# Kernel optimization log

Hardware: AMD Instinct MI355X
Metric: run time of the kernel (lower is better)

Reference implementation:

```python
import jax, jax.numpy as jnp
import numpy as np

HIDDEN = 1024
HEADS = 16
HEAD_DIM = HIDDEN // HEADS  # 64
MLP_HIDDEN = int(HIDDEN * 4.0)  # 4096
B, L = 2, 2048
EPS_LN = 1e-6
EPS_RMS = 1e-6


def setup_inputs() -> dict:
    key = jax.random.key(0)
    ks = jax.random.split(key, 12)
    s = 0.02
    return {
        "x": jax.random.normal(ks[0], (B, L, HIDDEN), jnp.float32),
        "vec": jax.random.normal(ks[1], (B, HIDDEN), jnp.float32),
        "pe": jax.random.normal(ks[2], (1, 1, L, HEAD_DIM // 2, 2, 2), jnp.float32),
        "w_mod": jax.random.normal(ks[3], (HIDDEN, 3 * HIDDEN), jnp.float32) * s,
        "b_mod": jnp.zeros((3 * HIDDEN,), jnp.float32),
        "w1": jax.random.normal(ks[4], (HIDDEN, 3 * HIDDEN + MLP_HIDDEN), jnp.float32) * s,
        "b1": jnp.zeros((3 * HIDDEN + MLP_HIDDEN,), jnp.float32),
        "w_mlp": jax.random.normal(ks[5], (MLP_HIDDEN, HIDDEN), jnp.float32) * s,
        "b_mlp": jnp.zeros((HIDDEN,), jnp.float32),
        "w2": jax.random.normal(ks[6], (2 * HIDDEN, HIDDEN), jnp.float32) * s,
        "b2": jnp.zeros((HIDDEN,), jnp.float32),
        "q_scale": jnp.ones((HEAD_DIM,), jnp.float32),
        "k_scale": jnp.ones((HEAD_DIM,), jnp.float32),
    }


def _layernorm(x, eps=EPS_LN):
    m = jnp.mean(x, axis=-1, keepdims=True)
    v = jnp.mean(jnp.square(x - m), axis=-1, keepdims=True)
    return (x - m) * jax.lax.rsqrt(v + eps)


def _rmsnorm(x, scale, eps=EPS_RMS):
    rrms = jax.lax.rsqrt(jnp.mean(jnp.square(x), axis=-1, keepdims=True) + eps)
    return x * rrms * scale


def _apply_rope(t, pe):
    # t: [B,H,L,D]; pe: [1,1,L,D//2,2,2]
    t_ = t.reshape(*t.shape[:-1], -1, 1, 2)  # [B,H,L,D//2,1,2]
    out = pe[..., 0] * t_[..., 0] + pe[..., 1] * t_[..., 1]  # [B,H,L,D//2,2]
    return out.reshape(t.shape)


def reference(x, vec, pe, w_mod, b_mod, w1, b1, w_mlp, b_mlp, w2, b2, q_scale, k_scale):
    # adaLN modulation: silu(vec) -> Dense(3*dim) -> shift, scale, gate
    mod = (jax.nn.silu(vec) @ w_mod + b_mod)[:, None, :]  # [B,1,3H]
    shift, scale, gate = jnp.split(mod, 3, axis=-1)
    x_mod = (1.0 + scale) * _layernorm(x) + shift
    # fused QKV + MLP projection
    h = x_mod @ w1 + b1  # [B,L,3H+MH]
    qkv, mlp = h[..., : 3 * HIDDEN], h[..., 3 * HIDDEN :]
    qkv = qkv.reshape(x.shape[0], x.shape[1], 3, HEADS, HEAD_DIM)
    qkv = jnp.transpose(qkv, (2, 0, 3, 1, 4))  # [3,B,H,L,D]
    q, k, v = qkv[0], qkv[1], qkv[2]
    # QK-RMSNorm per head-dim
    q = _rmsnorm(q, q_scale)
    k = _rmsnorm(k, k_scale)
    # RoPE
    q = _apply_rope(q, pe)
    k = _apply_rope(k, pe)
    # attention
    scores = jnp.einsum("bhqd,bhkd->bhqk", q, k) * (HEAD_DIM ** -0.5)
    probs = jax.nn.softmax(scores, axis=-1)
    attn = jnp.einsum("bhqk,bhkd->bhqd", probs, v)
    attn = jnp.transpose(attn, (0, 2, 1, 3)).reshape(x.shape[0], x.shape[1], HIDDEN)
    # mlp branch (Dense with tanh activation per source) + fused output proj
    mlp_out = jnp.tanh(mlp @ w_mlp + b_mlp)
    out = jnp.concatenate([attn, mlp_out], axis=-1) @ w2 + b2
    return x + gate * out
```

## Files before the change

kernel.cpp:

```cpp
#include <hip/hip_runtime.h>
#include <stdint.h>


#define HID  1024
#define NH   16
#define HD   64
#define MLP  4096
#define D1   7168
#define DQKV 3072
#define DCAT 2048
#define BB   2
#define LL   2048
#define TOK  4096

typedef __attribute__((ext_vector_type(8))) short    bf16x8;
typedef __attribute__((ext_vector_type(4))) float    f32x4;
typedef __attribute__((ext_vector_type(4))) unsigned int u32x4;

__device__ __forceinline__ float b2f(unsigned short u) {
    unsigned int v = ((unsigned int)u) << 16;
    float f; __builtin_memcpy(&f, &v, 4); return f;
}
__device__ __forceinline__ unsigned short f2b(float f) {
    unsigned int v; __builtin_memcpy(&v, &f, 4);
    unsigned int r = (v + 0x7FFFu + ((v >> 16) & 1u)) >> 16;
    return (unsigned short)r;
}
__device__ __forceinline__ unsigned int pkbf2(float a, float b) {
    unsigned int ua, ub;
    __builtin_memcpy(&ua, &a, 4); __builtin_memcpy(&ub, &b, 4);
    return ((ua + 0x8000u) >> 16) | ((ub + 0x8000u) & 0xFFFF0000u);
}
__device__ __forceinline__ void gl_lds16(const unsigned short* g, unsigned short* l) {
    __builtin_amdgcn_global_load_lds(
        (const __attribute__((address_space(1))) unsigned int*)(g),
        (__attribute__((address_space(3))) unsigned int*)(l), 16, 0, 0);
}

__global__ void k_transpose_cvt(const float* __restrict__ in,
                                unsigned short* __restrict__ out, int R, int C) {
    __shared__ float tile[32][33];
    int bx = blockIdx.x, by = blockIdx.y;
    int tx = threadIdx.x, ty = threadIdx.y;
    #pragma unroll
    for (int i = 0; i < 4; i++) {
        int r = by * 32 + ty + i * 8;
        int c = bx * 32 + tx;
        tile[ty + i * 8][tx] = in[(size_t)r * C + c];
    }
    __syncthreads();
    #pragma unroll
    for (int i = 0; i < 4; i++) {
        int ro = bx * 32 + ty + i * 8;
        int co = by * 32 + tx;
        out[(size_t)ro * R + co] = f2b(tile[tx][ty + i * 8]);
    }
}

__global__ void k_mod(const float* __restrict__ vec,
                      const float* __restrict__ w_mod,
                      const float* __restrict__ b_mod,
                      float* __restrict__ mod) {
    __shared__ float sv[HID];
    __shared__ float red[8][32];
    int b = blockIdx.y, t = threadIdx.x;
    for (int j = t; j < HID; j += 256) {
        float v = vec[b * HID + j];
        sv[j] = v / (1.0f + __expf(-v));
    }
    __syncthreads();
    int n0 = blockIdx.x * 32;
    int on = t & 31, ks = t >> 5;
    float acc = 0.f;
    const float* wp = w_mod + (size_t)(ks * 128) * 3072 + n0 + on;
    #pragma unroll 4
    for (int k = 0; k < 128; k++) acc += sv[ks * 128 + k] * wp[(size_t)k * 3072];
    red[ks][on] = acc;
    __syncthreads();
    if (t < 32) {
        float s = 0.f;
        #pragma unroll
        for (int i = 0; i < 8; i++) s += red[i][t];
        mod[b * 3072 + n0 + t] = s + b_mod[n0 + t];
    }
}

__global__ void k_lnmod(const float* __restrict__ x,
                        const float* __restrict__ mod,
                        unsigned short* __restrict__ xmod) {
    int tok = blockIdx.x;
    int t = threadIdx.x;
    int b = tok >> 11;
    float4 v4 = *(const float4*)(x + (size_t)tok * HID + t * 4);
    float v0 = v4.x, v1 = v4.y, v2 = v4.z, v3 = v4.w;
    float s  = v0 + v1 + v2 + v3;
    float sq = v0*v0 + v1*v1 + v2*v2 + v3*v3;
    for (int off = 1; off < 64; off <<= 1) {
        s  += __shfl_xor(s,  off);
        sq += __shfl_xor(sq, off);
    }
    __shared__ float ls[4], lq[4];
    int w = t >> 6;
    if ((t & 63) == 0) { ls[w] = s; lq[w] = sq; }
    __syncthreads();
    s  = ls[0] + ls[1] + ls[2] + ls[3];
    sq = lq[0] + lq[1] + lq[2] + lq[3];
    float mean = s * (1.0f / HID);
    float var  = sq * (1.0f / HID) - mean * mean;
    float rstd = rsqrtf(var + 1e-6f);
    const float* mb = mod + b * 3072;
    float y[4] = {v0, v1, v2, v3};
    unsigned short r[4];
    #pragma unroll
    for (int j = 0; j < 4; j++) {
        int col = t * 4 + j;
        float nval = (y[j] - mean) * rstd;
        r[j] = f2b((1.0f + mb[1024 + col]) * nval + mb[col]);
    }
    unsigned int o0 = (unsigned int)r[0] | ((unsigned int)r[1] << 16);
    unsigned int o1 = (unsigned int)r[2] | ((unsigned int)r[3] << 16);
    *(uint2*)(xmod + (size_t)tok * HID + t * 4) = make_uint2(o0, o1);
}

template<int EPI>
__global__ __launch_bounds__(256) void k_gemm(
    const unsigned short* __restrict__ A, int lda,
    const unsigned short* __restrict__ Bt, int ldb,
    const float* __restrict__ bias,
    unsigned short* __restrict__ C, float* __restrict__ Cf, int ldc,
    int K,
    const float* __restrict__ xin,
    const float* __restrict__ mod) {
    __shared__ alignas(16) unsigned short As[128 * 64];
    __shared__ alignas(16) unsigned short Bs[128 * 64];
    int t = threadIdx.x;
    int bm = blockIdx.x, bn = blockIdx.y;
    int lane = t & 63, wave = t >> 6;
    int wm = (wave >> 1) * 64, wn = (wave & 1) * 64;
    int ln = lane & 15, kq = lane >> 4;
    int ln7 = ln & 7;

    f32x4 acc[4][4];
    #pragma unroll
    for (int i = 0; i < 4; i++)
        #pragma unroll
        for (int j = 0; j < 4; j++) acc[i][j] = {0.f, 0.f, 0.f, 0.f};

    int sr  = t >> 3;
    int scg = (t & 7) ^ (sr & 7);
    const unsigned short* Ab = A  + (size_t)(bm * 128) * lda;
    const unsigned short* Bb = Bt + (size_t)(bn * 128) * ldb;

    int ksplit = K / gridDim.z;
    int kbeg = blockIdx.z * ksplit, kend = kbeg + ksplit;

    for (int k0 = kbeg; k0 < kend; k0 += 64) {
        __syncthreads();
        #pragma unroll
        for (int c = 0; c < 4; c++) {
            gl_lds16(Ab + (size_t)(c * 32 + sr) * lda + k0 + scg * 8, &As[c * 2048 + t * 8]);
            gl_lds16(Bb + (size_t)(c * 32 + sr) * ldb + k0 + scg * 8, &Bs[c * 2048 + t * 8]);
        }
        __syncthreads();
        #pragma unroll
        for (int ks = 0; ks < 2; ks++) {
            int slot = ((ks * 4 + kq) ^ ln7) * 8;
            bf16x8 af[4], bfr[4];
            #pragma unroll
            for (int i = 0; i < 4; i++)
                af[i] = *(const bf16x8*)(&As[(wm + i * 16 + ln) * 64 + slot]);
            #pragma unroll
            for (int j = 0; j < 4; j++)
                bfr[j] = *(const bf16x8*)(&Bs[(wn + j * 16 + ln) * 64 + slot]);
            #pragma unroll
            for (int i = 0; i < 4; i++)
                #pragma unroll
                for (int j = 0; j < 4; j++)
                    acc[i][j] = __builtin_amdgcn_mfma_f32_16x16x32_bf16(af[i], bfr[j], acc[i][j], 0, 0, 0);
        }
    }

    #pragma unroll
    for (int i = 0; i < 4; i++) {
        #pragma unroll
        for (int j = 0; j < 4; j++) {
            int col = bn * 128 + wn + j * 16 + ln;
            float bv = (EPI == 3) ? 0.f : bias[col];
            #pragma unroll
            for (int r = 0; r < 4; r++) {
                int row = bm * 128 + wm + i * 16 + kq * 4 + r;
                float v = acc[i][j][r] + bv;
                if (EPI == 0) {
                    C[(size_t)row * ldc + col] = f2b(v);
                } else if (EPI == 1) {
                    C[(size_t)row * ldc + col] = f2b(tanhf(v));
                } else if (EPI == 2) {
                    int b = row >> 11;
                    Cf[(size_t)row * ldc + col] =
                        xin[(size_t)row * HID + col] + mod[b * 3072 + 2048 + col] * v;
                } else {
                    Cf[((size_t)blockIdx.z * TOK + row) * ldc + col] = v;
                }
            }
        }
    }
}

__global__ __launch_bounds__(256) void k_red1(const float* __restrict__ part,
                                              const float* __restrict__ bias,
                                              unsigned short* __restrict__ cat) {
    int idx = blockIdx.x * 256 + threadIdx.x;
    int row = idx >> 8;
    int c4  = (idx & 255) * 4;
    float4 p0 = *(const float4*)(part + (size_t)row * HID + c4);
    float4 p1 = *(const float4*)(part + ((size_t)TOK + row) * HID + c4);
    float4 bv = *(const float4*)(bias + c4);
    float a0 = tanhf(p0.x + p1.x + bv.x);
    float a1 = tanhf(p0.y + p1.y + bv.y);
    float a2 = tanhf(p0.z + p1.z + bv.z);
    float a3 = tanhf(p0.w + p1.w + bv.w);
    *(uint2*)(&cat[(size_t)row * DCAT + HID + c4]) =
        make_uint2(pkbf2(a0, a1), pkbf2(a2, a3));
}

__global__ __launch_bounds__(256) void k_red2(const float* __restrict__ part,
                                              const float* __restrict__ bias,
                                              const float* __restrict__ x,
                                              const float* __restrict__ mod,
                                              float* __restrict__ out) {
    int idx = blockIdx.x * 256 + threadIdx.x;
    int row = idx >> 8;
    int c4  = (idx & 255) * 4;
    int b = row >> 11;
    float4 p0 = *(const float4*)(part + (size_t)row * HID + c4);
    float4 p1 = *(const float4*)(part + ((size_t)TOK + row) * HID + c4);
    float4 bv = *(const float4*)(bias + c4);
    float4 gv = *(const float4*)(mod + b * 3072 + 2048 + c4);
    float4 xv = *(const float4*)(x + (size_t)row * HID + c4);
    float4 o;
    o.x = xv.x + gv.x * (p0.x + p1.x + bv.x);
    o.y = xv.y + gv.y * (p0.y + p1.y + bv.y);
    o.z = xv.z + gv.z * (p0.z + p1.z + bv.z);
    o.w = xv.w + gv.w * (p0.w + p1.w + bv.w);
    *(float4*)(out + (size_t)row * HID + c4) = o;
}

__global__ void k_qkrope(unsigned short* __restrict__ h,
                         const float* __restrict__ pe,
                         const float* __restrict__ q_scale,
                         const float* __restrict__ k_scale) {
    int tok = blockIdx.x;
    int l = tok & (LL - 1);
    int t = threadIdx.x;
    int lane = t & 63, wave = t >> 6;
    int hh = wave * 4 + (lane >> 4);
    int d0 = (lane & 15) * 4;
    unsigned short* row = h + (size_t)tok * D1;
    int i0 = d0 >> 1;
    const float* peb = pe + ((size_t)l * 32 + i0) * 4;
    float4 e0 = *(const float4*)(peb);
    float4 e1 = *(const float4*)(peb + 4);
    #pragma unroll
    for (int qk = 0; qk < 2; qk++) {
        unsigned short* p = row + qk * HID + hh * HD + d0;
        const float* sc = (qk == 0 ? q_scale : k_scale) + d0;
        uint2 qv = *(const uint2*)p;
        float v0 = b2f((unsigned short)(qv.x & 0xFFFF)), v1 = b2f((unsigned short)(qv.x >> 16));
        float v2 = b2f((unsigned short)(qv.y & 0xFFFF)), v3 = b2f((unsigned short)(qv.y >> 16));
        float ssq = v0*v0 + v1*v1 + v2*v2 + v3*v3;
        ssq += __shfl_xor(ssq, 1, 16);
        ssq += __shfl_xor(ssq, 2, 16);
        ssq += __shfl_xor(ssq, 4, 16);
        ssq += __shfl_xor(ssq, 8, 16);
        float rr = rsqrtf(ssq * (1.0f / HD) + 1e-6f);
        if (qk == 0) rr *= 0.18033688011112042f;
        v0 *= rr * sc[0];
        v1 *= rr * sc[1];
        v2 *= rr * sc[2];
        v3 *= rr * sc[3];
        float o0 = e0.x*v0 + e0.y*v1;
        float o1 = e0.z*v0 + e0.w*v1;
        float o2 = e1.x*v2 + e1.y*v3;
        float o3 = e1.z*v2 + e1.w*v3;
        *(uint2*)p = make_uint2(pkbf2(o0, o1), pkbf2(o2, o3));
    }
}

#define KT 64
#define LDP 72
__global__ __launch_bounds__(256) void k_attn(const unsigned short* __restrict__ h,
                                              unsigned short* __restrict__ cat) {
    __shared__ unsigned short Ks[KT * LDP];
    __shared__ unsigned short Vt[HD * LDP];
    __shared__ unsigned short Ps[4 * 16 * LDP];
    int t = threadIdx.x;
    int bx = blockIdx.x;
    int bh = blockIdx.y;
    int b = bh >> 4, hh = bh & 15;
    int lane = t & 63, w = t >> 6;
    int ln = lane & 15, quad = lane >> 4;
    const unsigned short* hb = h + (size_t)b * LL * D1;

    bf16x8 qf[2];
    {
        const unsigned short* qbase = hb + (size_t)(bx * 64 + w * 16) * D1 + hh * HD;
        #pragma unroll
        for (int ks = 0; ks < 2; ks++)
            qf[ks] = *(const bf16x8*)(qbase + (size_t)ln * D1 + ks * 32 + quad * 8);
    }

    f32x4 O[4];
    #pragma unroll
    for (int vn = 0; vn < 4; vn++) O[vn] = {0.f, 0.f, 0.f, 0.f};
    float m_ = -1e30f, l_ = 0.f;

    unsigned short* Psw = Ps + w * 16 * LDP;

    int skey = t >> 2, sdc = (t & 3) * 16;
    int p2 = (t & 31) * 2, db = (t >> 5) * 8;

    for (int kb = 0; kb < LL / KT; kb++) {
        __syncthreads();
        {
            const unsigned short* kbase = hb + (size_t)(kb * KT) * D1 + HID + hh * HD;
            u32x4 ka = *(const u32x4*)(kbase + (size_t)skey * D1 + sdc);
            u32x4 kc = *(const u32x4*)(kbase + (size_t)skey * D1 + sdc + 8);
            *(u32x4*)(&Ks[skey * LDP + sdc]) = ka;
            *(u32x4*)(&Ks[skey * LDP + sdc + 8]) = kc;
            const unsigned short* vbase = hb + (size_t)(kb * KT) * D1 + 2 * HID + hh * HD;
            u32x4 va = *(const u32x4*)(vbase + (size_t)p2 * D1 + db);
            u32x4 vb = *(const u32x4*)(vbase + (size_t)(p2 + 1) * D1 + db);
            #pragma unroll
            for (int j = 0; j < 8; j++) {
                unsigned int lo = (j & 1) ? (va[j >> 1] >> 16) : (va[j >> 1] & 0xFFFFu);
                unsigned int hi = (j & 1) ? (vb[j >> 1] >> 16) : (vb[j >> 1] & 0xFFFFu);
                *(unsigned int*)(&Vt[(db + j) * LDP + p2]) = lo | (hi << 16);
            }
        }
        __syncthreads();

        f32x4 st[4];
        #pragma unroll
        for (int kt = 0; kt < 4; kt++) {
            st[kt] = {0.f, 0.f, 0.f, 0.f};
            #pragma unroll
            for (int ks = 0; ks < 2; ks++) {
                bf16x8 kf = *(const bf16x8*)(&Ks[(kt * 16 + ln) * LDP + ks * 32 + quad * 8]);
                st[kt] = __builtin_amdgcn_mfma_f32_16x16x32_bf16(kf, qf[ks], st[kt], 0, 0, 0);
            }
        }

        {
            float p[16];
            float mx = -1e30f;
            #pragma unroll
            for (int kt = 0; kt < 4; kt++)
                #pragma unroll
                for (int r = 0; r < 4; r++) {
                    float v = st[kt][r];
                    p[kt * 4 + r] = v;
                    mx = fmaxf(mx, v);
                }
            mx = fmaxf(mx, __shfl_xor(mx, 16));
            mx = fmaxf(mx, __shfl_xor(mx, 32));
            float mnew = fmaxf(m_, mx);
            float alpha = __builtin_amdgcn_exp2f(m_ - mnew);
            m_ = mnew;
            float sum = 0.f;
            #pragma unroll
            for (int i = 0; i < 16; i++) {
                float e = __builtin_amdgcn_exp2f(p[i] - mnew);
                p[i] = e;
                sum += e;
            }
            sum += __shfl_xor(sum, 16);
            sum += __shfl_xor(sum, 32);
            l_ = l_ * alpha + sum;
            #pragma unroll
            for (int vn = 0; vn < 4; vn++)
                #pragma unroll
                for (int r = 0; r < 4; r++) O[vn][r] *= alpha;
            #pragma unroll
            for (int kt = 0; kt < 4; kt++) {
                unsigned long long pk =
                    (unsigned long long)pkbf2(p[kt*4+0], p[kt*4+1])
                  | ((unsigned long long)pkbf2(p[kt*4+2], p[kt*4+3]) << 32);
                *(unsigned long long*)(&Psw[ln * LDP + kt * 16 + quad * 4]) = pk;
            }
        }

        #pragma unroll
        for (int kt2 = 0; kt2 < 2; kt2++) {
            bf16x8 pb = *(const bf16x8*)(&Psw[ln * LDP + kt2 * 32 + quad * 8]);
            #pragma unroll
            for (int vn = 0; vn < 4; vn++) {
                bf16x8 vf = *(const bf16x8*)(&Vt[(vn * 16 + ln) * LDP + kt2 * 32 + quad * 8]);
                O[vn] = __builtin_amdgcn_mfma_f32_16x16x32_bf16(vf, pb, O[vn], 0, 0, 0);
            }
        }
    }

    {
        float rl = 1.0f / l_;
        size_t row = (size_t)(b * LL + bx * 64 + w * 16 + ln);
        #pragma unroll
        for (int vn = 0; vn < 4; vn++) {
            #pragma unroll
            for (int r2 = 0; r2 < 4; r2 += 2) {
                unsigned int pk = pkbf2(O[vn][r2] * rl, O[vn][r2 + 1] * rl);
                *(unsigned int*)(&cat[row * DCAT + hh * HD + vn * 16 + quad * 4 + r2]) = pk;
            }
        }
    }
}

extern "C" void kernel_launch(void* const* d_in, const int* in_sizes, int n_in,
                              void* d_out, int out_size, void* d_ws, size_t ws_size,
                              hipStream_t stream) {
    const float* x       = (const float*)d_in[0];
    const float* vec     = (const float*)d_in[1];
    const float* pe      = (const float*)d_in[2];
    const float* w_mod   = (const float*)d_in[3];
    const float* b_mod   = (const float*)d_in[4];
    const float* w1      = (const float*)d_in[5];
    const float* b1      = (const float*)d_in[6];
    const float* w_mlp   = (const float*)d_in[7];
    const float* b_mlp   = (const float*)d_in[8];
    const float* w2      = (const float*)d_in[9];
    const float* b2      = (const float*)d_in[10];
    const float* q_scale = (const float*)d_in[11];
    const float* k_scale = (const float*)d_in[12];
    float* out = (float*)d_out;

    char* ws = (char*)d_ws;
    size_t off = 0;
    float* mod = (float*)(ws + off);                     off += 6144 * 4;
    unsigned short* xmod  = (unsigned short*)(ws + off); off += (size_t)TOK * HID * 2;
    unsigned short* h     = (unsigned short*)(ws + off); off += (size_t)TOK * D1 * 2;
    unsigned short* cat   = (unsigned short*)(ws + off); off += (size_t)TOK * DCAT * 2;
    unsigned short* w1T   = (unsigned short*)(ws + off); off += (size_t)D1 * HID * 2;
    unsigned short* wmlpT = (unsigned short*)(ws + off); off += (size_t)HID * MLP * 2;
    unsigned short* w2T   = (unsigned short*)(ws + off); off += (size_t)HID * DCAT * 2;
    float* part = (float*)(ws + off);                    off += (size_t)2 * TOK * HID * 4;

    k_transpose_cvt<<<dim3(D1 / 32, HID / 32), dim3(32, 8), 0, stream>>>(w1, w1T, HID, D1);
    k_transpose_cvt<<<dim3(HID / 32, MLP / 32), dim3(32, 8), 0, stream>>>(w_mlp, wmlpT, MLP, HID);
    k_transpose_cvt<<<dim3(HID / 32, DCAT / 32), dim3(32, 8), 0, stream>>>(w2, w2T, DCAT, HID);

    k_mod<<<dim3(96, BB), 256, 0, stream>>>(vec, w_mod, b_mod, mod);
    k_lnmod<<<TOK, 256, 0, stream>>>(x, mod, xmod);

    k_gemm<0><<<dim3(TOK / 128, D1 / 128), 256, 0, stream>>>(
        xmod, HID, w1T, HID, b1, h, nullptr, D1, HID, nullptr, nullptr);

    k_qkrope<<<TOK, 256, 0, stream>>>(h, pe, q_scale, k_scale);

    k_attn<<<dim3(LL / 64, BB * NH), 256, 0, stream>>>(h, cat);

    k_gemm<3><<<dim3(TOK / 128, HID / 128, 2), 256, 0, stream>>>(
        h + DQKV, D1, wmlpT, MLP, b_mlp, nullptr, part, HID, MLP, nullptr, nullptr);
    k_red1<<<TOK * HID / 1024, 256, 0, stream>>>(part, b_mlp, cat);

    k_gemm<3><<<dim3(TOK / 128, HID / 128, 2), 256, 0, stream>>>(
        cat, DCAT, w2T, DCAT, b2, nullptr, part, HID, DCAT, nullptr, nullptr);
    k_red2<<<TOK * HID / 1024, 256, 0, stream>>>(part, b2, x, mod, out);
}
```

Measured before the change: 417.9 us.

## Add 256x256-tile pipelined GEMM for the fused QKV+MLP projection

Replaces the 128x128 generic GEMM for the largest projection (4096x7168x1024) with a dedicated 512-thread kernel using 256x256 output tiles, double-buffered LDS staged by direct global-to-LDS loads, and interleaved half-tile prefetch with MFMA quadrants. It also adds an XCD-aware workgroup swizzle and setprio around MFMA blocks. The goal is more data reuse per tile and overlap of memory loads with matrix math. In exchange it raises register and LDS pressure and leaves fewer workgroups in the grid (448), which may limit occupancy.

```diff
diff --git a/kernel.cpp b/kernel.cpp
--- a/kernel.cpp
+++ b/kernel.cpp
@@ -202,6 +202,145 @@
                     Cf[((size_t)blockIdx.z * TOK + row) * ldc + col] = v;
                 }
             }
+        }
+    }
+}
+
+#define KD   1024
+#define NT16 16
+
+#define STAGE_A2(BUF, H, KO) do { \
+    const unsigned short* s_ = Ab + (size_t)((H) * 128 + sr) * KD + (KO) + scg8; \
+    gl_lds16(s_,            &As[BUF][H][t * 8]); \
+    gl_lds16(s_ + 64 * KD,  &As[BUF][H][4096 + t * 8]); \
+  } while (0)
+
+#define STAGE_B2(BUF, H, KO) do { \
+    const unsigned short* s_ = Bb + (size_t)((H) * 128 + sr) * KD + (KO) + scg8; \
+    gl_lds16(s_,            &Bs[BUF][H][t * 8]); \
+    gl_lds16(s_ + 64 * KD,  &Bs[BUF][H][4096 + t * 8]); \
+  } while (0)
+
+#define LDA_H(DST, BUF, MH) do { \
+    _Pragma("unroll") \
+    for (int i_ = 0; i_ < 4; i_++) { \
+      const unsigned short* ap_ = &As[BUF][wmh][(MH) * 4096 + i_ * 1024 + lnx64]; \
+      DST[i_][0] = *(const bf16x8*)(ap_ + sA0); \
+      DST[i_][1] = *(const bf16x8*)(ap_ + sA1); \
+    } \
+  } while (0)
+
+#define LDB_H(DST, BUF, NH) do { \
+    _Pragma("unroll") \
+    for (int j_ = 0; j_ < 2; j_++) { \
+      const unsigned short* bp_ = &Bs[BUF][wnh][bro + (NH) * 2048 + j_ * 1024 + lnx64]; \
+      DST[j_][0] = *(const bf16x8*)(bp_ + sA0); \
+      DST[j_][1] = *(const bf16x8*)(bp_ + sA1); \
+    } \
+  } while (0)
+
+#define MMQ(AF, BF, IG0, JG0) do { \
+    __builtin_amdgcn_s_setprio(1); \
+    _Pragma("unroll") \
+    for (int ks_ = 0; ks_ < 2; ks_++) \
+      _Pragma("unroll") \
+      for (int i_ = 0; i_ < 4; i_++) \
+        _Pragma("unroll") \
+        for (int j_ = 0; j_ < 2; j_++) \
+          acc[(IG0) + i_][(JG0) + j_] = __builtin_amdgcn_mfma_f32_16x16x32_bf16( \
+              AF[i_][ks_], BF[j_][ks_], acc[(IG0) + i_][(JG0) + j_], 0, 0, 0); \
+    __builtin_amdgcn_s_setprio(0); \
+  } while (0)
+
+__global__ __launch_bounds__(512, 2) void k_gemm256(
+    const unsigned short* __restrict__ A,
+    const unsigned short* __restrict__ Bt,
+    const float* __restrict__ bias,
+    unsigned short* __restrict__ C) {
+    __shared__ alignas(16) unsigned short As[2][2][128 * 64];
+    __shared__ alignas(16) unsigned short Bs[2][2][128 * 64];
+
+    int wg  = blockIdx.x;
+    int cpx = gridDim.x >> 3;
+    int swz = (wg & 7) * cpx + (wg >> 3);
+    int bm = swz & 15;
+    int bn = swz >> 4;
+
+    int t = threadIdx.x;
+    int lane = t & 63, wid = t >> 6;
+    int wmh = wid >> 2;
+    int wnq = wid & 3;
+    int wnh = wnq >> 1;
+    int bro = (wnq & 1) * 4096;
+    int ln = lane & 15, kq = lane >> 4, ln7 = lane & 7;
+    int lnx64 = ln * 64;
+    int sA0 = ((0 + kq) ^ ln7) * 8;
+    int sA1 = ((4 + kq) ^ ln7) * 8;
+
+    int sr   = t >> 3;
+    int scg8 = (((t & 7) ^ (sr & 7))) * 8;
+
+    const unsigned short* Ab = A  + (size_t)(bm * 256) * KD;
+    const unsigned short* Bb = Bt + (size_t)(bn * 256) * KD;
+
+    f32x4 acc[8][4];
+    #pragma unroll
+    for (int i = 0; i < 8; i++)
+        #pragma unroll
+        for (int j = 0; j < 4; j++) acc[i][j] = {0.f, 0.f, 0.f, 0.f};
+
+    STAGE_A2(0, 0, 0);  STAGE_A2(0, 1, 0);
+    STAGE_B2(0, 0, 0);  STAGE_B2(0, 1, 0);
+    STAGE_A2(1, 0, 64); STAGE_A2(1, 1, 64);
+    asm volatile("s_waitcnt vmcnt(4)" ::: "memory");
+    __builtin_amdgcn_sched_barrier(0);
+    __builtin_amdgcn_s_barrier();
+
+    bf16x8 afA[4][2], afB[4][2], bf0[2][2], bf1[2][2];
+
+    for (int tau = 0; tau < NT16; ++tau) {
+        const int q  = tau & 1;
+        const int k0 = tau << 6;
+        LDA_H(afA, q, 0);
+        LDB_H(bf0, q, 0);
+        if (tau + 1 < NT16) STAGE_B2(q ^ 1, 0, k0 + 64);
+        __builtin_amdgcn_s_barrier();
+        asm volatile("s_waitcnt lgkmcnt(0)" ::: "memory");
+        __builtin_amdgcn_sched_barrier(0);
+        MMQ(afA, bf0, 0, 0);
+        __builtin_amdgcn_s_barrier();
+        LDA_H(afB, q, 1);
+        LDB_H(bf1, q, 1);
+        if (tau + 1 < NT16) STAGE_B2(q ^ 1, 1, k0 + 64);
+        __builtin_amdgcn_s_barrier();
+        asm volatile("s_waitcnt lgkmcnt(0)" ::: "memory");
+        __builtin_amdgcn_sched_barrier(0);
+        MMQ(afA, bf1, 0, 2);
+        __builtin_amdgcn_s_barrier();
+        if (tau + 2 < NT16) STAGE_A2(q, 0, k0 + 128);
+        MMQ(afB, bf1, 4, 2);
+        __builtin_amdgcn_s_barrier();
+        if (tau + 2 < NT16) STAGE_A2(q, 1, k0 + 128);
+        MMQ(afB, bf0, 4, 0);
+        if (tau + 2 < NT16) {
+            asm volatile("s_waitcnt vmcnt(4)" ::: "memory");
+        } else if (tau + 1 < NT16) {
+            asm volatile("s_waitcnt vmcnt(0)" ::: "memory");
+        }
+        __builtin_amdgcn_sched_barrier(0);
+        __builtin_amdgcn_s_barrier();
+    }
+
+    #pragma unroll
+    for (int jg = 0; jg < 4; jg++) {
+        int col = bn * 256 + wnq * 64 + jg * 16 + ln;
+        float bv = bias[col];
+        #pragma unroll
+        for (int ig = 0; ig < 8; ig++) {
+            int row = bm * 256 + wmh * 128 + ig * 16 + kq * 4;
+            #pragma unroll
+            for (int r = 0; r < 4; r++)
+                C[(size_t)(row + r) * D1 + col] = f2b(acc[ig][jg][r] + bv);
         }
     }
 }
@@ -450,8 +589,7 @@
     k_mod<<<dim3(96, BB), 256, 0, stream>>>(vec, w_mod, b_mod, mod);
     k_lnmod<<<TOK, 256, 0, stream>>>(x, mod, xmod);
 
-    k_gemm<0><<<dim3(TOK / 128, D1 / 128), 256, 0, stream>>>(
-        xmod, HID, w1T, HID, b1, h, nullptr, D1, HID, nullptr, nullptr);
+    k_gemm256<<<dim3((TOK / 256) * (D1 / 256)), dim3(512), 0, stream>>>(xmod, w1T, b1, h);
 
     k_qkrope<<<TOK, 256, 0, stream>>>(h, pe, q_scale, k_scale);
 
```

Result: no change. 415.1 us (-0.7%).
